# Optimization experiments

Hardware: AMD Instinct MI355X
Metric: run time of the kernel (lower is better)

The kernel has to match this reference:

```python
import jax, jax.numpy as jnp
import numpy as np

N = 50000
E = 800000
IN = 256
HEADS = 8
C = 32  # out_size // heads
OUT = HEADS * C
NEG_SLOPE = 0.2
LN_EPS = 1e-5


def setup_inputs() -> dict:
    key = jax.random.key(0)
    ks = jax.random.split(key, 6)
    x = jax.random.normal(ks[0], (N, IN), dtype=jnp.float32)
    edge_index = jax.random.randint(ks[1], (2, E), 0, N, dtype=jnp.int64)
    W = jax.random.normal(ks[2], (IN, OUT), dtype=jnp.float32) / np.sqrt(IN)
    att_src = jax.random.normal(ks[3], (HEADS, C), dtype=jnp.float32) / np.sqrt(C)
    att_dst = jax.random.normal(ks[4], (HEADS, C), dtype=jnp.float32) / np.sqrt(C)
    bias = jnp.zeros((OUT,), dtype=jnp.float32)
    ln_gamma = jnp.ones((OUT,), dtype=jnp.float32)
    ln_beta = jnp.zeros((OUT,), dtype=jnp.float32)
    return {"x": x, "edge_index": edge_index, "W": W, "att_src": att_src,
            "att_dst": att_dst, "bias": bias, "ln_gamma": ln_gamma, "ln_beta": ln_beta}


def _gat_layer(x, src, dst, W, att_src, att_dst, bias, ln_gamma, ln_beta):
    n = x.shape[0]
    h = (x @ W).reshape(n, HEADS, C)                      # [N,H,C]
    a_src = jnp.sum(h * att_src[None], axis=-1)           # [N,H]
    a_dst = jnp.sum(h * att_dst[None], axis=-1)           # [N,H]
    e = a_src[src] + a_dst[dst]                           # [Etot,H]
    e = jnp.where(e > 0, e, NEG_SLOPE * e)                # LeakyReLU(0.2)
    # segment softmax over incoming edges of each dst node
    emax = jax.lax.stop_gradient(jax.ops.segment_max(e, dst, num_segments=n))
    ex = jnp.exp(e - emax[dst])
    denom = jax.ops.segment_sum(ex, dst, num_segments=n)
    alpha = ex / denom[dst]                               # [Etot,H]
    msg = h[src] * alpha[:, :, None]                      # [Etot,H,C]
    out = jax.ops.segment_sum(msg, dst, num_segments=n).reshape(n, OUT) + bias
    # LayerNorm
    mu = jnp.mean(out, axis=-1, keepdims=True)
    var = jnp.var(out, axis=-1, keepdims=True)
    out = (out - mu) * jax.lax.rsqrt(var + LN_EPS) * ln_gamma + ln_beta
    return jax.nn.relu(out)


def reference(x, edge_index, W, att_src, att_dst, bias, ln_gamma, ln_beta):
    n = x.shape[0]
    loops = jnp.arange(n, dtype=edge_index.dtype)
    src = jnp.concatenate([edge_index[0], loops])  # PyG GATConv adds self-loops
    dst = jnp.concatenate([edge_index[1], loops])
    return _gat_layer(x, src, dst, W, att_src, att_dst, bias, ln_gamma, ln_beta)
```

## Files before the change

kernel.cpp:

```cpp
#include <hip/hip_runtime.h>

#define NEG 0.2f
#define ELLW 64

typedef __attribute__((ext_vector_type(8))) __bf16 bf16x8;
typedef __attribute__((ext_vector_type(4))) float f32x4;

__device__ __forceinline__ unsigned short f2bf(float f) {
    unsigned int u = __float_as_uint(f);
    u += 0x7FFFu + ((u >> 16) & 1u);
    return (unsigned short)(u >> 16);
}

__global__ __launch_bounds__(256) void prep_kernel(const float* __restrict__ W,
                                                   unsigned short* __restrict__ Wt,
                                                   int* __restrict__ len, int N) {
    int n = blockIdx.x, k = threadIdx.x;
    Wt[n * 256 + k] = f2bf(W[k * 256 + n]);
    int idx = n * 256 + k;
    if (idx < N) len[idx] = 0;
}

struct SmemGemm { unsigned short A[64][40]; unsigned short B[256][40]; };
struct SmemEpi  { float asrc[64][9]; float adst[64][9]; };
union SmemU { SmemGemm g; SmemEpi e; };

__global__ __launch_bounds__(256) void gemm_ell(const float* __restrict__ x,
                                                const unsigned short* __restrict__ Wt,
                                                unsigned short* __restrict__ h,
                                                const float* __restrict__ att_src,
                                                const float* __restrict__ att_dst,
                                                float* __restrict__ a_src,
                                                float* __restrict__ a_dst, int nrows, int G,
                                                const int* __restrict__ ei,
                                                int* __restrict__ len,
                                                int* __restrict__ ell, int E) {
    __shared__ SmemU sm;

    int bx = blockIdx.x;
    int EB = (E + 2047) >> 11;
    int EBint = EB < (G >> 1) ? EB : (G >> 1);
    int isell, widx;
    if (bx < 3 * EBint) {
        if ((bx % 3) == 2) { isell = 1; widx = bx / 3; }
        else               { isell = 0; widx = bx - bx / 3; }
    } else {
        int rest = bx - 3 * EBint;
        int gleft = G - 2 * EBint;
        if (rest < gleft) { isell = 0; widx = 2 * EBint + rest; }
        else              { isell = 1; widx = EBint + (rest - gleft); }
    }

    if (isell) {
        int base = widx * 2048 + threadIdx.x;
        int s0 = -1, s1 = -1, s2 = -1, s3 = -1, s4 = -1, s5 = -1, s6 = -1, s7 = -1;
        int d0 = 0, d1 = 0, d2 = 0, d3 = 0, d4 = 0, d5 = 0, d6 = 0, d7 = 0;
#define ELOAD(K, SK, DK) { int e_ = base + (K) * 256; \
        if (e_ < E) { SK = ei[e_]; DK = ei[E + e_]; } }
        ELOAD(0, s0, d0) ELOAD(1, s1, d1) ELOAD(2, s2, d2) ELOAD(3, s3, d3)
        ELOAD(4, s4, d4) ELOAD(5, s5, d5) ELOAD(6, s6, d6) ELOAD(7, s7, d7)
#undef ELOAD
        int t0 = 0, t1 = 0, t2 = 0, t3 = 0, t4 = 0, t5 = 0, t6 = 0, t7 = 0;
        if (s0 >= 0) t0 = atomicAdd(&len[d0], 1);
        if (s1 >= 0) t1 = atomicAdd(&len[d1], 1);
        if (s2 >= 0) t2 = atomicAdd(&len[d2], 1);
        if (s3 >= 0) t3 = atomicAdd(&len[d3], 1);
        if (s4 >= 0) t4 = atomicAdd(&len[d4], 1);
        if (s5 >= 0) t5 = atomicAdd(&len[d5], 1);
        if (s6 >= 0) t6 = atomicAdd(&len[d6], 1);
        if (s7 >= 0) t7 = atomicAdd(&len[d7], 1);
        if (s0 >= 0 && t0 < ELLW) ell[d0 * ELLW + t0] = s0;
        if (s1 >= 0 && t1 < ELLW) ell[d1 * ELLW + t1] = s1;
        if (s2 >= 0 && t2 < ELLW) ell[d2 * ELLW + t2] = s2;
        if (s3 >= 0 && t3 < ELLW) ell[d3 * ELLW + t3] = s3;
        if (s4 >= 0 && t4 < ELLW) ell[d4 * ELLW + t4] = s4;
        if (s5 >= 0 && t5 < ELLW) ell[d5 * ELLW + t5] = s5;
        if (s6 >= 0 && t6 < ELLW) ell[d6 * ELLW + t6] = s6;
        if (s7 >= 0 && t7 < ELLW) ell[d7 * ELLW + t7] = s7;
        return;
    }

    int t = threadIdx.x;
    int lane = t & 63, wave = t >> 6;
    int row0 = widx * 64;

    f32x4 acc[4][4] = {};

    for (int kk = 0; kk < 8; ++kk) {
        int k0 = kk * 32;
        {
            int r = t >> 2, cg = (t & 3) * 8;
            int gr = row0 + r;
            float4 v0 = make_float4(0.f, 0.f, 0.f, 0.f), v1 = v0;
            if (gr < nrows) {
                const float* p = x + (size_t)gr * 256 + k0 + cg;
                v0 = *(const float4*)p;
                v1 = *(const float4*)(p + 4);
            }
            uint4 av;
            av.x = (unsigned int)f2bf(v0.x) | ((unsigned int)f2bf(v0.y) << 16);
            av.y = (unsigned int)f2bf(v0.z) | ((unsigned int)f2bf(v0.w) << 16);
            av.z = (unsigned int)f2bf(v1.x) | ((unsigned int)f2bf(v1.y) << 16);
            av.w = (unsigned int)f2bf(v1.z) | ((unsigned int)f2bf(v1.w) << 16);
            *(uint4*)&sm.g.A[r][cg] = av;
        }
        {
            const uint4* src = (const uint4*)(Wt + (size_t)t * 256 + k0);
            uint4 b0 = src[0], b1 = src[1], b2 = src[2], b3 = src[3];
            *(uint4*)&sm.g.B[t][0]  = b0;
            *(uint4*)&sm.g.B[t][8]  = b1;
            *(uint4*)&sm.g.B[t][16] = b2;
            *(uint4*)&sm.g.B[t][24] = b3;
        }
        __syncthreads();

        int fr = lane & 15, fk = (lane >> 4) * 8;
        bf16x8 a[4];
#pragma unroll
        for (int mi = 0; mi < 4; ++mi) a[mi] = *(const bf16x8*)&sm.g.A[mi * 16 + fr][fk];
#pragma unroll
        for (int ni = 0; ni < 4; ++ni) {
            bf16x8 b = *(const bf16x8*)&sm.g.B[wave * 64 + ni * 16 + fr][fk];
#pragma unroll
            for (int mi = 0; mi < 4; ++mi)
                acc[mi][ni] = __builtin_amdgcn_mfma_f32_16x16x32_bf16(a[mi], b, acc[mi][ni], 0, 0, 0);
        }
        __syncthreads();
    }

    int cr = (lane >> 4) * 4;
    int cc = lane & 15;
#pragma unroll
    for (int mi = 0; mi < 4; ++mi)
#pragma unroll
        for (int ni = 0; ni < 4; ++ni)
#pragma unroll
            for (int r = 0; r < 4; ++r) {
                int row = row0 + mi * 16 + cr + r;
                int col = wave * 64 + ni * 16 + cc;
                if (row < nrows) h[(size_t)row * 256 + col] = f2bf(acc[mi][ni][r]);
            }

    float avs[4], avd[4];
#pragma unroll
    for (int ni = 0; ni < 4; ++ni) {
        int col = wave * 64 + ni * 16 + cc;
        avs[ni] = att_src[col];
        avd[ni] = att_dst[col];
    }
#pragma unroll
    for (int mi = 0; mi < 4; ++mi)
#pragma unroll
        for (int r = 0; r < 4; ++r) {
            float s0 = acc[mi][0][r] * avs[0] + acc[mi][1][r] * avs[1];
            float s1 = acc[mi][2][r] * avs[2] + acc[mi][3][r] * avs[3];
            float d0 = acc[mi][0][r] * avd[0] + acc[mi][1][r] * avd[1];
            float d1 = acc[mi][2][r] * avd[2] + acc[mi][3][r] * avd[3];
#pragma unroll
            for (int o = 1; o < 16; o <<= 1) {
                s0 += __shfl_xor(s0, o, 64);
                s1 += __shfl_xor(s1, o, 64);
                d0 += __shfl_xor(d0, o, 64);
                d1 += __shfl_xor(d1, o, 64);
            }
            if (cc == 0) {
                int row = mi * 16 + cr + r;
                sm.e.asrc[row][wave * 2 + 0] = s0;
                sm.e.asrc[row][wave * 2 + 1] = s1;
                sm.e.adst[row][wave * 2 + 0] = d0;
                sm.e.adst[row][wave * 2 + 1] = d1;
            }
        }
    __syncthreads();
    for (int idx = t; idx < 512; idx += 256) {
        int row = idx >> 3, hd = idx & 7;
        if (row0 + row < nrows) {
            a_src[(size_t)(row0 + row) * 8 + hd] = sm.e.asrc[row][hd];
            a_dst[(size_t)(row0 + row) * 8 + hd] = sm.e.adst[row][hd];
        }
    }
}

__device__ __forceinline__ void fma8(f32x4& a0, f32x4& a1, float al, uint4 u) {
    a0[0] = fmaf(al, __uint_as_float(u.x << 16),         a0[0]);
    a0[1] = fmaf(al, __uint_as_float(u.x & 0xffff0000u), a0[1]);
    a0[2] = fmaf(al, __uint_as_float(u.y << 16),         a0[2]);
    a0[3] = fmaf(al, __uint_as_float(u.y & 0xffff0000u), a0[3]);
    a1[0] = fmaf(al, __uint_as_float(u.z << 16),         a1[0]);
    a1[1] = fmaf(al, __uint_as_float(u.z & 0xffff0000u), a1[1]);
    a1[2] = fmaf(al, __uint_as_float(u.w << 16),         a1[2]);
    a1[3] = fmaf(al, __uint_as_float(u.w & 0xffff0000u), a1[3]);
}

__global__ __launch_bounds__(256, 6) void agg_kernel(const unsigned short* __restrict__ h,
                                                     const float* __restrict__ a_src,
                                                     const float* __restrict__ a_dst,
                                                     const int* __restrict__ len,
                                                     const int* __restrict__ ell,
                                                     const float* __restrict__ bias,
                                                     const float* __restrict__ gamma,
                                                     const float* __restrict__ beta,
                                                     float* __restrict__ out, int N) {
    __shared__ float alL[4][ELLW][8];

    int lane = threadIdx.x & 63, wave = threadIdx.x >> 6;
    int i = blockIdx.x * 4 + wave;
    if (i >= N) return;

    volatile float (*al)[8] = alL[wave];

    int deg = len[i];
    deg = deg < ELLW ? deg : ELLW;
    int dm1 = deg - 1;

    int sreg = (lane < deg) ? ell[i * ELLW + lane] : 0;

    int hh = lane & 7, jj = lane >> 3;
    float adh = a_dst[i * 8 + hh];
    float es = a_src[i * 8 + hh] + adh;
    es = es > 0.f ? es : NEG * es;
    float selfexp = __expf(es);

    float sum = (jj == 0) ? selfexp : 0.f;
    for (int jb = 0; jb < deg; jb += 8) {
        int j = jb + jj;
        int jc = j < deg ? j : dm1;
        int s = __shfl(sreg, jc, 64);
        float e = a_src[s * 8 + hh] + adh;
        e = e > 0.f ? e : NEG * e;
        float v = __expf(e);
        if (j < deg) {
            al[j][hh] = v;
            sum += v;
        }
    }
    sum += __shfl_xor(sum, 8, 64);
    sum += __shfl_xor(sum, 16, 64);
    sum += __shfl_xor(sum, 32, 64);
    float ginv = 1.0f / sum;

    __builtin_amdgcn_wave_barrier();

    int sub = lane >> 5, l5 = lane & 31;
    int c0 = l5 * 8;
    int hl = l5 >> 2;
    float gv = __shfl(ginv, hl, 64);
    float sv = __shfl(selfexp, hl, 64);

    f32x4 a0 = {0.f, 0.f, 0.f, 0.f}, a1 = {0.f, 0.f, 0.f, 0.f};
    if (deg > 0) {
#define P2LOAD(jb, AL, U) { \
        int j_ = (jb) + sub; \
        int jc_ = j_ < deg ? j_ : dm1; \
        int s_ = __shfl(sreg, jc_, 64); \
        AL = (j_ < deg ? al[jc_][hl] : 0.f) * gv; \
        U = *(const uint4*)(h + (size_t)s_ * 256 + c0); }

        float alA, alB;
        uint4 uA, uB;
        P2LOAD(0, alA, uA)
        P2LOAD(2, alB, uB)
        int jb = 0;
        for (; jb + 4 < deg; jb += 4) {
            fma8(a0, a1, alA, uA); P2LOAD(jb + 4, alA, uA)
            fma8(a0, a1, alB, uB); P2LOAD(jb + 6, alB, uB)
        }
        fma8(a0, a1, alA, uA);
        fma8(a0, a1, alB, uB);
#undef P2LOAD
    }
    {
        float alphaS = (sub == 1) ? sv * gv : 0.f;
        uint4 us = *(const uint4*)(h + (size_t)i * 256 + c0);
        fma8(a0, a1, alphaS, us);
    }
#pragma unroll
    for (int k = 0; k < 4; ++k) {
        a0[k] += __shfl_xor(a0[k], 32, 64);
        a1[k] += __shfl_xor(a1[k], 32, 64);
    }

    float4 b0 = *(const float4*)(bias + c0);
    float4 b1 = *(const float4*)(bias + c0 + 4);
    float o0 = a0[0] + b0.x, o1 = a0[1] + b0.y, o2 = a0[2] + b0.z, o3 = a0[3] + b0.w;
    float o4 = a1[0] + b1.x, o5 = a1[1] + b1.y, o6 = a1[2] + b1.z, o7 = a1[3] + b1.w;

    float s1 = o0 + o1 + o2 + o3 + o4 + o5 + o6 + o7;
    float s2 = o0 * o0 + o1 * o1 + o2 * o2 + o3 * o3
             + o4 * o4 + o5 * o5 + o6 * o6 + o7 * o7;
#pragma unroll
    for (int off = 16; off >= 1; off >>= 1) {
        s1 += __shfl_xor(s1, off, 64);
        s2 += __shfl_xor(s2, off, 64);
    }
    float mean = s1 * (1.f / 256.f);
    float var = s2 * (1.f / 256.f) - mean * mean;
    float rstd = rsqrtf(var + 1e-5f);

    float4 g0 = *(const float4*)(gamma + c0);
    float4 g1 = *(const float4*)(gamma + c0 + 4);
    float4 t0 = *(const float4*)(beta + c0);
    float4 t1 = *(const float4*)(beta + c0 + 4);

    f32x4 w0, w1;
    w0[0] = fmaxf((o0 - mean) * rstd * g0.x + t0.x, 0.f);
    w0[1] = fmaxf((o1 - mean) * rstd * g0.y + t0.y, 0.f);
    w0[2] = fmaxf((o2 - mean) * rstd * g0.z + t0.z, 0.f);
    w0[3] = fmaxf((o3 - mean) * rstd * g0.w + t0.w, 0.f);
    w1[0] = fmaxf((o4 - mean) * rstd * g1.x + t1.x, 0.f);
    w1[1] = fmaxf((o5 - mean) * rstd * g1.y + t1.y, 0.f);
    w1[2] = fmaxf((o6 - mean) * rstd * g1.z + t1.z, 0.f);
    w1[3] = fmaxf((o7 - mean) * rstd * g1.w + t1.w, 0.f);

    float* op = out + (size_t)i * 256 + c0;
    if (sub == 0) *(f32x4*)op       = w0;
    else          *(f32x4*)(op + 4) = w1;
}

extern "C" void kernel_launch(void* const* d_in, const int* in_sizes, int n_in,
                              void* d_out, int out_size, void* d_ws, size_t ws_size,
                              hipStream_t stream) {
    const float* x       = (const float*)d_in[0];
    const int*   ei      = (const int*)d_in[1];
    const float* W       = (const float*)d_in[2];
    const float* att_src = (const float*)d_in[3];
    const float* att_dst = (const float*)d_in[4];
    const float* bias    = (const float*)d_in[5];
    const float* gamma   = (const float*)d_in[6];
    const float* beta    = (const float*)d_in[7];

    int N = in_sizes[0] / 256;
    int E = in_sizes[1] / 2;
    int G = (N + 63) / 64;
    int EB = (E + 2047) / 2048;

    char* ws = (char*)d_ws;
    size_t off = 0;
    auto alloc = [&](size_t bytes) -> void* {
        void* p = ws + off;
        off += (bytes + 255) & ~(size_t)255;
        return p;
    };
    unsigned short* Wt     = (unsigned short*)alloc((size_t)256 * 256 * 2);
    unsigned short* h      = (unsigned short*)alloc((size_t)N * 256 * 2);
    float*          a_src_ = (float*)alloc((size_t)N * 8 * 4);
    float*          a_dst_ = (float*)alloc((size_t)N * 8 * 4);
    int*            len    = (int*)alloc((size_t)N * 4);
    int*            ell    = (int*)alloc((size_t)N * ELLW * 4);

    prep_kernel<<<256, 256, 0, stream>>>(W, Wt, len, N);
    gemm_ell<<<G + EB, 256, 0, stream>>>(x, Wt, h, att_src, att_dst, a_src_, a_dst_, N, G,
                                         ei, len, ell, E);
    agg_kernel<<<(N + 3) / 4, 256, 0, stream>>>(h, a_src_, a_dst_, len, ell, bias, gamma, beta,
                                                (float*)d_out, N);
}
```

Measured before the change: 243.2 us.

## Fuse softmax weight computation into aggregation loop, drop LDS alpha pass

```diff
diff --git a/kernel.cpp b/kernel.cpp
--- a/kernel.cpp
+++ b/kernel.cpp
@@ -192,98 +192,97 @@
     a1[3] = fmaf(al, __uint_as_float(u.w & 0xffff0000u), a1[3]);
 }
 
-__global__ __launch_bounds__(256, 6) void agg_kernel(const unsigned short* __restrict__ h,
-                                                     const float* __restrict__ a_src,
-                                                     const float* __restrict__ a_dst,
-                                                     const int* __restrict__ len,
-                                                     const int* __restrict__ ell,
-                                                     const float* __restrict__ bias,
-                                                     const float* __restrict__ gamma,
-                                                     const float* __restrict__ beta,
-                                                     float* __restrict__ out, int N) {
-    __shared__ float alL[4][ELLW][8];
-
+__global__ __launch_bounds__(256) void agg_kernel(const unsigned short* __restrict__ h,
+                                                  const float* __restrict__ a_src,
+                                                  const float* __restrict__ a_dst,
+                                                  const int* __restrict__ len,
+                                                  const int* __restrict__ ell,
+                                                  const float* __restrict__ bias,
+                                                  const float* __restrict__ gamma,
+                                                  const float* __restrict__ beta,
+                                                  float* __restrict__ out, int N) {
     int lane = threadIdx.x & 63, wave = threadIdx.x >> 6;
     int i = blockIdx.x * 4 + wave;
     if (i >= N) return;
 
-    volatile float (*al)[8] = alL[wave];
-
     int deg = len[i];
     deg = deg < ELLW ? deg : ELLW;
     int dm1 = deg - 1;
 
     int sreg = (lane < deg) ? ell[i * ELLW + lane] : 0;
 
-    int hh = lane & 7, jj = lane >> 3;
-    float adh = a_dst[i * 8 + hh];
-    float es = a_src[i * 8 + hh] + adh;
-    es = es > 0.f ? es : NEG * es;
-    float selfexp = __expf(es);
-
-    float sum = (jj == 0) ? selfexp : 0.f;
-    for (int jb = 0; jb < deg; jb += 8) {
-        int j = jb + jj;
-        int jc = j < deg ? j : dm1;
-        int s = __shfl(sreg, jc, 64);
-        float e = a_src[s * 8 + hh] + adh;
-        e = e > 0.f ? e : NEG * e;
-        float v = __expf(e);
-        if (j < deg) {
-            al[j][hh] = v;
-            sum += v;
-        }
-    }
-    sum += __shfl_xor(sum, 8, 64);
-    sum += __shfl_xor(sum, 16, 64);
-    sum += __shfl_xor(sum, 32, 64);
-    float ginv = 1.0f / sum;
-
-    __builtin_amdgcn_wave_barrier();
-
     int sub = lane >> 5, l5 = lane & 31;
     int c0 = l5 * 8;
     int hl = l5 >> 2;
-    float gv = __shfl(ginv, hl, 64);
-    float sv = __shfl(selfexp, hl, 64);
+
+    float adh = a_dst[i * 8 + hl];
+    float es = a_src[i * 8 + hl] + adh;
+    es = es > 0.f ? es : NEG * es;
+    float selfexp = __expf(es);
 
     f32x4 a0 = {0.f, 0.f, 0.f, 0.f}, a1 = {0.f, 0.f, 0.f, 0.f};
+    float denom = (sub == 0) ? selfexp : 0.f;
+
     if (deg > 0) {
-#define P2LOAD(jb, AL, U) { \
+#define PLOAD(jb, AV, U) { \
         int j_ = (jb) + sub; \
         int jc_ = j_ < deg ? j_ : dm1; \
         int s_ = __shfl(sreg, jc_, 64); \
-        AL = (j_ < deg ? al[jc_][hl] : 0.f) * gv; \
+        AV = (j_ < deg) ? a_src[(size_t)s_ * 8 + hl] : -1e30f; \
         U = *(const uint4*)(h + (size_t)s_ * 256 + c0); }
 
-        float alA, alB;
+        float avA, avB;
         uint4 uA, uB;
-        P2LOAD(0, alA, uA)
-        P2LOAD(2, alB, uB)
+        PLOAD(0, avA, uA)
+        PLOAD(2, avB, uB)
         int jb = 0;
         for (; jb + 4 < deg; jb += 4) {
-            fma8(a0, a1, alA, uA); P2LOAD(jb + 4, alA, uA)
-            fma8(a0, a1, alB, uB); P2LOAD(jb + 6, alB, uB)
-        }
-        fma8(a0, a1, alA, uA);
-        fma8(a0, a1, alB, uB);
-#undef P2LOAD
+            {
+                float e = avA + adh; e = e > 0.f ? e : NEG * e;
+                float w = __expf(e); denom += w;
+                uint4 uc = uA;
+                PLOAD(jb + 4, avA, uA)
+                fma8(a0, a1, w, uc);
+            }
+            {
+                float e = avB + adh; e = e > 0.f ? e : NEG * e;
+                float w = __expf(e); denom += w;
+                uint4 uc = uB;
+                PLOAD(jb + 6, avB, uB)
+                fma8(a0, a1, w, uc);
+            }
+        }
+        {
+            float e = avA + adh; e = e > 0.f ? e : NEG * e;
+            float w = __expf(e); denom += w;
+            fma8(a0, a1, w, uA);
+        }
+        {
+            float e = avB + adh; e = e > 0.f ? e : NEG * e;
+            float w = __expf(e); denom += w;
+            fma8(a0, a1, w, uB);
+        }
+#undef PLOAD
     }
     {
-        float alphaS = (sub == 1) ? sv * gv : 0.f;
+        float wS = (sub == 1) ? selfexp : 0.f;
         uint4 us = *(const uint4*)(h + (size_t)i * 256 + c0);
-        fma8(a0, a1, alphaS, us);
+        fma8(a0, a1, wS, us);
     }
 #pragma unroll
     for (int k = 0; k < 4; ++k) {
         a0[k] += __shfl_xor(a0[k], 32, 64);
         a1[k] += __shfl_xor(a1[k], 32, 64);
     }
+    denom += __shfl_xor(denom, 32, 64);
+    float ginv = 1.0f / denom;
 
     float4 b0 = *(const float4*)(bias + c0);
     float4 b1 = *(const float4*)(bias + c0 + 4);
-    float o0 = a0[0] + b0.x, o1 = a0[1] + b0.y, o2 = a0[2] + b0.z, o3 = a0[3] + b0.w;
-    float o4 = a1[0] + b1.x, o5 = a1[1] + b1.y, o6 = a1[2] + b1.z, o7 = a1[3] + b1.w;
+    float o0 = a0[0] * ginv + b0.x, o1 = a0[1] * ginv + b0.y;
+    float o2 = a0[2] * ginv + b0.z, o3 = a0[3] * ginv + b0.w;
+    float o4 = a1[0] * ginv + b1.x, o5 = a1[1] * ginv + b1.y;
+    float o6 = a1[2] * ginv + b1.z, o7 = a1[3] * ginv + b1.w;
 
     float s1 = o0 + o1 + o2 + o3 + o4 + o5 + o6 + o7;
     float s2 = o0 * o0 + o1 * o1 + o2 * o2 + o3 * o3
```

Measured after the change: 243.3 us. About the same (+0.1%).
